# Performance work log

Measured on AMD Instinct MI355X. Metric: run time of the kernel, lower is better.

## Reference

```python
import jax, jax.numpy as jnp
import numpy as np
import math

D_MODEL, N_HEADS, BATCH, SEQ = 1024, 16, 2, 2048
D_HEAD = D_MODEL // N_HEADS


def setup_inputs() -> dict:
    key = jax.random.key(0)
    ks = jax.random.split(key, 5)
    w = lambda k: jax.random.normal(k, (D_MODEL, D_MODEL), jnp.float32) * 0.02
    return {
        "X": jax.random.normal(ks[0], (BATCH, SEQ, D_MODEL), jnp.float32),
        "W_q": w(ks[1]),
        "W_k": w(ks[2]),
        "W_v": w(ks[3]),
        "W_o": w(ks[4]),
        "g_q": jnp.ones((D_MODEL,), jnp.float32),
        "b_q": jnp.zeros((D_MODEL,), jnp.float32),
        "g_k": jnp.ones((D_MODEL,), jnp.float32),
        "b_k": jnp.zeros((D_MODEL,), jnp.float32),
        "cache_k": jnp.zeros((BATCH, N_HEADS, SEQ, D_HEAD), jnp.float32),
        "cache_v": jnp.zeros((BATCH, N_HEADS, SEQ, D_HEAD), jnp.float32),
        "start_pos": 0,
    }


def _layernorm(x, g, b, eps=1e-5):
    mu = jnp.mean(x, axis=-1, keepdims=True)
    xc = x - mu
    var = jnp.mean(xc * xc, axis=-1, keepdims=True)
    return xc * jax.lax.rsqrt(var + eps) * g + b


def reference(X, W_q, W_k, W_v, W_o, g_q, b_q, g_k, b_k, cache_k, cache_v, start_pos):
    batch, N, d_model = X.shape
    H = cache_k.shape[1]
    dh = d_model // H

    # QK-normed projections (torch Linear: x @ W^T)
    XQ = _layernorm(X @ W_q.T, g_q, b_q)
    XK = _layernorm(X @ W_k.T, g_k, b_k)
    XV = X @ W_v.T
    split = lambda t: t.reshape(batch, N, H, dh).transpose(0, 2, 1, 3)  # [b,h,n,d]
    XQ, XK, XV = split(XQ), split(XK), split(XV)

    # KV-cache scatter update, then slice to valid prefix (start_pos is static)
    cache_k = jax.lax.dynamic_update_slice(cache_k, XK, (0, 0, start_pos, 0))
    cache_v = jax.lax.dynamic_update_slice(cache_v, XV, (0, 0, start_pos, 0))
    M = start_pos + N
    K = cache_k[:, :, :M]
    V = cache_v[:, :, :M]

    logits = jnp.einsum('bhnd,bhmd->bhnm', XQ, K) / math.sqrt(dh)  # [b,h,N,M]

    # causal mask on the freshly written block [start_pos:M]
    tril = jnp.tril(jnp.ones((N, N), bool))
    full_mask = jnp.concatenate([jnp.ones((N, start_pos), bool), tril], axis=1)  # [N,M]
    logits = jnp.where(full_mask[None, None], logits, -jnp.inf)

    # selective forget-mask bias built from relu'd head-0 logits
    S = jax.nn.relu(logits[:, 0])               # relu(-inf) -> 0, matches torch
    S = S.at[..., 0].set(0.0)                   # zero first column
    S = S * (1.0 - jnp.eye(N, dtype=S.dtype))   # zero diagonal (valid since start_pos==0)
    S = jnp.roll(S, 1, axis=-2)                 # shift rows down by one
    S = S.at[..., 0, :].set(0.0)
    F_mask = jnp.cumsum(S, axis=-2)             # [b,N,M]

    logits = logits - F_mask[:, None]
    attn = jax.nn.softmax(logits, axis=-1)
    O = jnp.einsum('bhnm,bhmd->bhnd', attn, V)
    O = O.transpose(0, 2, 1, 3).reshape(batch, N, d_model)
    return O @ W_o.T
```

## Files before the change

kernel.cpp:

```cpp
#include <hip/hip_runtime.h>
#include <cstdint>
#include <cstddef>


typedef unsigned short u16;
typedef __attribute__((ext_vector_type(8))) __bf16 bf16x8;
typedef __attribute__((ext_vector_type(4))) float f32x4;

#define D_MODEL 1024
#define N_HEADS 16
#define BATCH   2
#define SEQ     2048
#define D_HEAD  64
#define ROWS    (BATCH*SEQ)
#define NSEG    64
#define SEGLEN  32
#define LOG2E   1.44269504f

static __device__ __forceinline__ u16 f2bf(float f){
  union { float f; uint32_t u; } v; v.f = f;
  uint32_t r = v.u + 0x7fffu + ((v.u >> 16) & 1u);
  return (u16)(r >> 16);
}
static __device__ __forceinline__ float bf2f(u16 h){
  union { uint32_t u; float f; } v; v.u = ((uint32_t)h) << 16;
  return v.f;
}
static __device__ __forceinline__ uint32_t pack2(float a, float b){
  uint32_t ua = __float_as_uint(a) + 0x8000u;
  uint32_t ub = __float_as_uint(b) + 0x8000u;
  return (ua >> 16) | (ub & 0xffff0000u);
}
#define GLDS(gp, lp) __builtin_amdgcn_global_load_lds( \
    (const __attribute__((address_space(1))) void*)(gp), \
    (__attribute__((address_space(3))) void*)(lp), 16, 0, 0)

__global__ void k_cast_all(const float* __restrict__ X,
                           u16* __restrict__ Xhi, u16* __restrict__ Xlo,
                           const float* __restrict__ Wq,
                           u16* __restrict__ Wqh, u16* __restrict__ Wql,
                           const float* __restrict__ Wk,
                           u16* __restrict__ Wkh, u16* __restrict__ Wkl,
                           const float* __restrict__ Wv, u16* __restrict__ Wvb,
                           const float* __restrict__ Wo, u16* __restrict__ Wob){
  int i = blockIdx.x*256 + threadIdx.x;
  if (i < 1572864){
    const float* src; u16 *dh, *dl; int base;
    if (i < 1048576){ src = X;  dh = Xhi; dl = Xlo; base = i; }
    else if (i < 1310720){ src = Wq; dh = Wqh; dl = Wql; base = i - 1048576; }
    else { src = Wk; dh = Wkh; dl = Wkl; base = i - 1310720; }
    float4 v = reinterpret_cast<const float4*>(src)[base];
    float vs[4] = {v.x, v.y, v.z, v.w};
    union { u16 s[4]; uint2 u; } uh, ul;
#pragma unroll
    for (int r=0;r<4;++r){
      uh.s[r] = f2bf(vs[r]);
      ul.s[r] = f2bf(vs[r] - bf2f(uh.s[r]));
    }
    reinterpret_cast<uint2*>(dh)[base] = uh.u;
    reinterpret_cast<uint2*>(dl)[base] = ul.u;
  } else {
    const float* src; u16* dst; int base;
    if (i < 1835008){ src = Wv; dst = Wvb; base = i - 1572864; }
    else { src = Wo; dst = Wob; base = i - 1835008; }
    float4 v = reinterpret_cast<const float4*>(src)[base];
    float vs[4] = {v.x, v.y, v.z, v.w};
    union { u16 s[4]; uint2 u; } uh;
#pragma unroll
    for (int r=0;r<4;++r) uh.s[r] = f2bf(vs[r]);
    reinterpret_cast<uint2*>(dst)[base] = uh.u;
  }
}

__global__ __launch_bounds__(256) void k_mega(
    const u16* __restrict__ Xhi, const u16* __restrict__ Xlo,
    const u16* __restrict__ Wh,  const u16* __restrict__ Wl,
    const u16* __restrict__ Wvb,
    float* __restrict__ C, float* __restrict__ Dlt, u16* __restrict__ Vt)
{
  __shared__ __align__(16) u16 smem[16384];
  const int bid = blockIdx.x;
  const int tid = threadIdx.x, wv = tid>>6, ln = tid&63;
  const int lane15 = ln&15, quad = ln>>4;
  const int wm = wv&1, wn = wv>>1;
  const int g = ln&7, sr = ln>>3;
  const int fs = lane15 & 7;
  f32x4 z = {0.f,0.f,0.f,0.f};
  u16* As = smem;
  u16* Bs = smem + 8192;

  if (bid < 128){
    const int cx = bid & 1;
    const int cy = (bid >> 1) & 31;
    const int cz = bid >> 6;
    const size_t rowBase = (size_t)cy*128;
    const size_t wbase = cx ? (size_t)1024*1024 : 0;
    const u16* Ap = cz ? Xlo : Xhi;
    const u16* Bp = (cz ? Wh : Wl) + wbase;
    f32x4 acc[4][2];
#pragma unroll
    for (int i=0;i<4;++i){ acc[i][0] = z; acc[i][1] = z; }
    for (int kt = 0; kt < 16; ++kt) {
      __syncthreads();
#pragma unroll
      for (int c = 0; c < 4; ++c) {
        int chunk = wv*4 + c, r = chunk*8 + sr;
        GLDS(Ap + (rowBase + r)*1024 + kt*64 + (g^sr)*8, As + chunk*512);
      }
#pragma unroll
      for (int c = 0; c < 2; ++c) {
        int chunk = wv*2 + c, r = chunk*8 + sr;
        GLDS(Bp + (size_t)r*1024 + kt*64 + (g^sr)*8, Bs + chunk*512);
      }
      __syncthreads();
#pragma unroll
      for (int k2=0;k2<2;++k2){
        bf16x8 af[4], bfb[2];
#pragma unroll
        for (int t=0;t<4;++t)
          af[t]  = *reinterpret_cast<const bf16x8*>(As + (wm*64 + t*16 + lane15)*64 + (((k2*4+quad)^fs)*8));
#pragma unroll
        for (int t=0;t<2;++t)
          bfb[t] = *reinterpret_cast<const bf16x8*>(Bs + (wn*32 + t*16 + lane15)*64 + (((k2*4+quad)^fs)*8));
#pragma unroll
        for (int i=0;i<4;++i)
#pragma unroll
          for (int j=0;j<2;++j)
            acc[i][j] = __builtin_amdgcn_mfma_f32_16x16x32_bf16(af[i], bfb[j], acc[i][j], 0,0,0);
      }
    }
#pragma unroll
    for (int i=0;i<4;++i){
      size_t row = rowBase + wm*64 + i*16 + quad*4;
#pragma unroll
      for (int j=0;j<2;++j){
        size_t col = (size_t)cx*64 + wn*32 + j*16 + lane15;
#pragma unroll
        for (int r=0;r<4;++r)
          atomicAdd(&Dlt[(row+r)*128 + col], acc[i][j][r]);
      }
    }
  } else if (bid < 640){
    const int idx = bid - 128;
    const size_t rowBase = (size_t)(idx>>4)*128, colBase = (size_t)(idx&15)*128;
    f32x4 acc[4][4];
#pragma unroll
    for (int i=0;i<4;++i)
#pragma unroll
      for (int j=0;j<4;++j) acc[i][j] = z;
    for (int kt = 0; kt < 16; ++kt) {
      __syncthreads();
#pragma unroll
      for (int c = 0; c < 4; ++c) {
        int chunk = wv*4 + c, r = chunk*8 + sr;
        GLDS(Xhi + (rowBase + r)*1024 + kt*64 + (g^sr)*8, As + chunk*512);
        GLDS(Wh  + (colBase + r)*1024 + kt*64 + (g^sr)*8, Bs + chunk*512);
      }
      __syncthreads();
#pragma unroll
      for (int k2=0;k2<2;++k2){
        bf16x8 af[4], bfb[4];
#pragma unroll
        for (int t=0;t<4;++t){
          af[t]  = *reinterpret_cast<const bf16x8*>(As + (wm*64 + t*16 + lane15)*64 + (((k2*4+quad)^fs)*8));
          bfb[t] = *reinterpret_cast<const bf16x8*>(Bs + (wn*64 + t*16 + lane15)*64 + (((k2*4+quad)^fs)*8));
        }
#pragma unroll
        for (int i=0;i<4;++i)
#pragma unroll
          for (int j=0;j<4;++j)
            acc[i][j] = __builtin_amdgcn_mfma_f32_16x16x32_bf16(af[i], bfb[j], acc[i][j], 0,0,0);
      }
    }
#pragma unroll
    for (int i=0;i<4;++i){
      size_t row = rowBase + wm*64 + i*16 + quad*4;
#pragma unroll
      for (int j=0;j<4;++j){
        size_t col = colBase + wn*64 + j*16 + lane15;
#pragma unroll
        for (int r=0;r<4;++r)
          C[(row+r)*2048 + col] = acc[i][j][r];
      }
    }
  } else {
    const int idx = bid - 640;
    const int bx = idx & 15, by = idx >> 4;
    const size_t rowBase = (size_t)by*128, colBase = (size_t)bx*64;
    f32x4 acc[4][2];
#pragma unroll
    for (int i=0;i<4;++i){ acc[i][0] = z; acc[i][1] = z; }
    for (int kt = 0; kt < 16; ++kt) {
      __syncthreads();
#pragma unroll
      for (int c = 0; c < 4; ++c) {
        int chunk = wv*4 + c, r = chunk*8 + sr;
        GLDS(Xhi + (rowBase + r)*1024 + kt*64 + (g^sr)*8, As + chunk*512);
      }
#pragma unroll
      for (int c = 0; c < 2; ++c) {
        int chunk = wv*2 + c, r = chunk*8 + sr;
        GLDS(Wvb + (colBase + r)*1024 + kt*64 + (g^sr)*8, Bs + chunk*512);
      }
      __syncthreads();
#pragma unroll
      for (int k2=0;k2<2;++k2){
        bf16x8 af[4], bfb[2];
#pragma unroll
        for (int t=0;t<4;++t)
          af[t]  = *reinterpret_cast<const bf16x8*>(As + (wm*64 + t*16 + lane15)*64 + (((k2*4+quad)^fs)*8));
#pragma unroll
        for (int t=0;t<2;++t)
          bfb[t] = *reinterpret_cast<const bf16x8*>(Bs + (wn*32 + t*16 + lane15)*64 + (((k2*4+quad)^fs)*8));
#pragma unroll
        for (int i=0;i<4;++i)
#pragma unroll
          for (int j=0;j<2;++j)
            acc[i][j] = __builtin_amdgcn_mfma_f32_16x16x32_bf16(af[i], bfb[j], acc[i][j], 0,0,0);
      }
    }
    __syncthreads();
#pragma unroll
    for (int i=0;i<4;++i){
      int nl = wm*64 + i*16 + quad*4;
#pragma unroll
      for (int j=0;j<2;++j){
        int dl = wn*32 + j*16 + lane15;
#pragma unroll
        for (int r=0;r<4;++r)
          smem[dl*136 + nl + r] = f2bf(acc[i][j][r]);
      }
    }
    __syncthreads();
    const int b = by >> 4;
    const int n0 = (by & 15) * 128;
    const int bh = b*N_HEADS + bx;
    const int d = tid >> 2, seg = tid & 3;
    u16* dst = Vt + ((size_t)(bh*64 + d))*SEQ + n0 + seg*32;
    const u16* srcl = smem + d*136 + seg*32;
#pragma unroll
    for (int k=0;k<4;++k)
      *reinterpret_cast<uint4*>(dst + k*8) = *reinterpret_cast<const uint4*>(srcl + k*8);
  }
}

__global__ __launch_bounds__(256) void k_ln_pack2(
    const float* __restrict__ C, const float* __restrict__ Dlt,
    const float* __restrict__ gq, const float* __restrict__ bq,
    const float* __restrict__ gk, const float* __restrict__ bk,
    u16* __restrict__ Qh, u16* __restrict__ Kh,
    u16* __restrict__ Q0l, u16* __restrict__ K0l)
{
  const int row = blockIdx.x;
  const int tid = threadIdx.x;
  const float* cr = C + (size_t)row*2048;
  float4 vq = reinterpret_cast<const float4*>(cr)[tid];
  float4 vk = reinterpret_cast<const float4*>(cr)[256 + tid];
  const int h = tid >> 4;
  if (h == 0){
    float4 dq = reinterpret_cast<const float4*>(Dlt + (size_t)row*128)[tid&15];
    vq.x+=dq.x; vq.y+=dq.y; vq.z+=dq.z; vq.w+=dq.w;
    float4 dk = reinterpret_cast<const float4*>(Dlt + (size_t)row*128 + 64)[tid&15];
    vk.x+=dk.x; vk.y+=dk.y; vk.z+=dk.z; vk.w+=dk.w;
  }
  float sq  = vq.x+vq.y+vq.z+vq.w;
  float s2q = vq.x*vq.x+vq.y*vq.y+vq.z*vq.z+vq.w*vq.w;
  float sk  = vk.x+vk.y+vk.z+vk.w;
  float s2k = vk.x*vk.x+vk.y*vk.y+vk.z*vk.z+vk.w*vk.w;
#pragma unroll
  for (int o=32;o;o>>=1){
    sq += __shfl_xor(sq,o);  s2q += __shfl_xor(s2q,o);
    sk += __shfl_xor(sk,o);  s2k += __shfl_xor(s2k,o);
  }
  __shared__ float red[4][4];
  if ((tid&63)==0){
    red[tid>>6][0]=sq; red[tid>>6][1]=s2q; red[tid>>6][2]=sk; red[tid>>6][3]=s2k;
  }
  __syncthreads();
  sq  = red[0][0]+red[1][0]+red[2][0]+red[3][0];
  s2q = red[0][1]+red[1][1]+red[2][1]+red[3][1];
  sk  = red[0][2]+red[1][2]+red[2][2]+red[3][2];
  s2k = red[0][3]+red[1][3]+red[2][3]+red[3][3];
  const float muq = sq*(1.f/D_MODEL);
  const float rsq = rsqrtf(s2q*(1.f/D_MODEL) - muq*muq + 1e-5f);
  const float muk = sk*(1.f/D_MODEL);
  const float rsk = rsqrtf(s2k*(1.f/D_MODEL) - muk*muk + 1e-5f);
  const int b = row >> 11, n = row & (SEQ-1);
  const int d0 = (tid & 15)*4;
  float4 gqv = reinterpret_cast<const float4*>(gq)[tid];
  float4 bqv = reinterpret_cast<const float4*>(bq)[tid];
  float4 gkv = reinterpret_cast<const float4*>(gk)[tid];
  float4 bkv = reinterpret_cast<const float4*>(bk)[tid];
  float xq[4] = {vq.x,vq.y,vq.z,vq.w}, xk[4] = {vk.x,vk.y,vk.z,vk.w};
  float gQ[4] = {gqv.x,gqv.y,gqv.z,gqv.w}, bQ[4] = {bqv.x,bqv.y,bqv.z,bqv.w};
  float gK[4] = {gkv.x,gkv.y,gkv.z,gkv.w}, bK[4] = {bkv.x,bkv.y,bkv.z,bkv.w};
  union { u16 s[4]; uint2 u; } qh, ql, kh, kl;
#pragma unroll
  for (int r=0;r<4;++r){
    float yq = (xq[r]-muq)*rsq*gQ[r] + bQ[r];
    qh.s[r] = f2bf(yq);
    ql.s[r] = f2bf(yq - bf2f(qh.s[r]));
    float yk = (xk[r]-muk)*rsk*gK[r] + bK[r];
    kh.s[r] = f2bf(yk);
    kl.s[r] = f2bf(yk - bf2f(kh.s[r]));
  }
  size_t dst = (((size_t)(b*N_HEADS + h))*SEQ + n)*D_HEAD + d0;
  *reinterpret_cast<uint2*>(Qh + dst) = qh.u;
  *reinterpret_cast<uint2*>(Kh + dst) = kh.u;
  if (h == 0){
    size_t dl = ((size_t)b*SEQ + n)*D_HEAD + d0;
    *reinterpret_cast<uint2*>(Q0l + dl) = ql.u;
    *reinterpret_cast<uint2*>(K0l + dl) = kl.u;
  }
}

__global__ __launch_bounds__(256) void k_s0(
    const u16* Qh, const u16* Q0l, const u16* Kh, const u16* K0l,
    float* __restrict__ S0, float* __restrict__ seg)
{
  const int b = blockIdx.z;
  const int bm = blockIdx.y;
  const int bn = blockIdx.x;
  const int tid = threadIdx.x;
  if (bn > bm){
    for (int t = tid; t < 512; t += 256)
      seg[((size_t)b*NSEG + bm*4 + (t>>7))*SEQ + bn*128 + (t&127)] = 0.f;
    return;
  }
  float* Sb = S0 + (size_t)b*SEQ*SEQ;
  __shared__ __align__(16) u16 smem[4*8192];
  const int wv = tid>>6, ln = tid&63;
  const int lane15 = ln&15, quad = ln>>4;
  const int wm = wv&1, wn = wv>>1;
  const int g = ln&7, sr = ln>>3;
  const int fs = lane15 & 7;
  const size_t rowBase = (size_t)bm*128, colBase = (size_t)bn*128;
  const u16* srcs[4] = {
    Qh  + ((size_t)b*N_HEADS*SEQ + rowBase)*D_HEAD,
    Q0l + ((size_t)b*SEQ + rowBase)*D_HEAD,
    Kh  + ((size_t)b*N_HEADS*SEQ + colBase)*D_HEAD,
    K0l + ((size_t)b*SEQ + colBase)*D_HEAD };
#pragma unroll
  for (int t=0;t<4;++t){
#pragma unroll
    for (int c=0;c<4;++c){
      int chunk = wv*4 + c, r = chunk*8 + sr;
      GLDS(srcs[t] + (size_t)r*64 + (g^sr)*8, smem + t*8192 + chunk*512);
    }
  }
  __syncthreads();
  f32x4 acc[4][4];
  f32x4 z = {0.f,0.f,0.f,0.f};
#pragma unroll
  for (int i=0;i<4;++i)
#pragma unroll
    for (int j=0;j<4;++j) acc[i][j] = z;
  const int Aidx[3] = {0, 0, 1};
  const int Bidx[3] = {2, 3, 2};
#pragma unroll
  for (int p = 0; p < 3; ++p){
    const u16* At = smem + Aidx[p]*8192;
    const u16* Bt = smem + Bidx[p]*8192;
#pragma unroll
    for (int k2=0;k2<2;++k2){
      bf16x8 af[4], bfb[4];
#pragma unroll
      for (int t=0;t<4;++t){
        af[t]  = *reinterpret_cast<const bf16x8*>(At + (wm*64 + t*16 + lane15)*64 + (((k2*4+quad)^fs)*8));
        bfb[t] = *reinterpret_cast<const bf16x8*>(Bt + (wn*64 + t*16 + lane15)*64 + (((k2*4+quad)^fs)*8));
      }
#pragma unroll
      for (int i=0;i<4;++i)
#pragma unroll
        for (int j=0;j<4;++j)
          acc[i][j] = __builtin_amdgcn_mfma_f32_16x16x32_bf16(af[i], bfb[j], acc[i][j], 0,0,0);
    }
  }
  float csum[2][4] = {{0.f,0.f,0.f,0.f},{0.f,0.f,0.f,0.f}};
#pragma unroll
  for (int i=0;i<4;++i){
#pragma unroll
    for (int j=0;j<4;++j){
#pragma unroll
      for (int r=0;r<4;++r){
        int jg = (int)rowBase + wm*64 + i*16 + quad*4 + r;
        int mg = (int)colBase + wn*64 + j*16 + lane15;
        float l = acc[i][j][r]*0.125f;
        float s = (mg >= 1 && mg < jg) ? fmaxf(l, 0.f) : 0.f;
        Sb[(size_t)jg*SEQ + mg] = s;
        csum[i>>1][j] += s;
      }
    }
  }
  __syncthreads();
  float* cs = (float*)smem;
#pragma unroll
  for (int h2=0;h2<2;++h2){
#pragma unroll
    for (int j=0;j<4;++j){
      float v = csum[h2][j];
      v += __shfl_xor(v, 16);
      v += __shfl_xor(v, 32);
      if (ln < 16) cs[(wm*2 + h2)*128 + wn*64 + j*16 + ln] = v;
    }
  }
  __syncthreads();
  for (int t = tid; t < 512; t += 256)
    seg[((size_t)b*NSEG + bm*4 + (t>>7))*SEQ + bn*128 + (t&127)] = cs[t];
}

__global__ void k_seg_apply(float* __restrict__ SF, const float* __restrict__ seg){
  int m = blockIdx.x*256 + threadIdx.x;
  int s = blockIdx.y, b = blockIdx.z;
  const float* sb = seg + (size_t)b*NSEG*SEQ;
  float run = 0.f;
  for (int t=0; t<s; ++t) run += sb[(size_t)t*SEQ + m];
  float* Sb = SF + (size_t)b*SEQ*SEQ;
  const int j0 = s*SEGLEN;
#pragma unroll 8
  for (int i=0;i<SEGLEN;++i){
    size_t idx = (size_t)(j0 + i)*SEQ + m;
    float t = Sb[idx];
    Sb[idx] = -run*LOG2E;
    run += (j0 + i > m) ? t : 0.f;
  }
}

__global__ __launch_bounds__(256, 4) void k_attn(
    const u16* __restrict__ Qh, const u16* __restrict__ Kh,
    const u16* __restrict__ Vt, const float* __restrict__ F,
    u16* __restrict__ Ob)
{
  __shared__ __align__(16) u16 Ks[2][64*64];
  __shared__ __align__(16) u16 Vs[2][64*64];
  const int h = blockIdx.x, b = blockIdx.z;
  const int nt = b ? (int)(gridDim.y - 1 - blockIdx.y) : (int)blockIdx.y;
  const int tid = threadIdx.x, wv = tid>>6, ln = tid&63;
  const int lane15 = ln&15, quad = ln>>4;
  const u16* Qbh = Qh + ((size_t)(b*N_HEADS + h))*SEQ*D_HEAD;
  const u16* Kbh = Kh + ((size_t)(b*N_HEADS + h))*SEQ*D_HEAD;
  const u16* Vbh = Vt + ((size_t)(b*N_HEADS + h))*D_HEAD*SEQ;
  const int n_loc = wv*16 + lane15;
  const int n_g = nt*64 + n_loc;
  const float* Frow = F + (size_t)b*SEQ*SEQ + (size_t)n_g*SEQ;
  const int swz = (ln&7) ^ ((ln>>3)&7);
  const int fswz = lane15 & 7;
  const int srow = ln>>3;

  bf16x8 qf[2];
#pragma unroll
  for (int kt=0; kt<2; ++kt)
    qf[kt] = *reinterpret_cast<const bf16x8*>(Qbh + (size_t)n_g*D_HEAD + kt*32 + quad*8);

  f32x4 z = {0.f,0.f,0.f,0.f};
  f32x4 psum = z;
  f32x4 acc_o[4];
#pragma unroll
  for (int no=0;no<4;++no) acc_o[no] = z;

  auto stage = [&](int mt, int buf){
#pragma unroll
    for (int c=0;c<2;++c){
      int chunk = wv*2 + c;
      int r = chunk*8 + srow;
      GLDS(Kbh + (size_t)(mt*64 + r)*D_HEAD + swz*8, &Ks[buf][chunk*512]);
      GLDS(Vbh + (size_t)r*SEQ + mt*64 + swz*8,      &Vs[buf][chunk*512]);
    }
  };
  stage(0, 0);
  f32x4 fvn[4];
#pragma unroll
  for (int ms=0; ms<4; ++ms)
    fvn[ms] = *reinterpret_cast<const f32x4*>(Frow + ms*16 + quad*4);
  const float c1 = 0.125f*LOG2E;

  for (int mt = 0; mt <= nt; ++mt) {
    const int cur = mt & 1;
    __syncthreads();
    if (mt < nt) stage(mt+1, 1-cur);
    f32x4 fv[4];
#pragma unroll
    for (int ms=0; ms<4; ++ms) fv[ms] = fvn[ms];
    if (mt < nt){
      const float* Fr1 = Frow + (mt+1)*64;
#pragma unroll
      for (int ms=0; ms<4; ++ms)
        fvn[ms] = *reinterpret_cast<const f32x4*>(Fr1 + ms*16 + quad*4);
    }
    f32x4 accs[4];
#pragma unroll
    for (int ms=0;ms<4;++ms) accs[ms] = z;
#pragma unroll
    for (int kt=0; kt<2; ++kt){
#pragma unroll
      for (int ms=0; ms<4; ++ms){
        bf16x8 a = *reinterpret_cast<const bf16x8*>(
            &Ks[cur][(ms*16 + lane15)*64 + (((kt*4 + quad) ^ fswz) * 8)]);
        accs[ms] = __builtin_amdgcn_mfma_f32_16x16x32_bf16(a, qf[kt], accs[ms], 0,0,0);
      }
    }
    const bool diag = (mt == nt);
    uint32_t pw[4][2];
#pragma unroll
    for (int ms=0; ms<4; ++ms){
      f32x4 t = accs[ms];
      float p[4];
#pragma unroll
      for (int r=0;r<4;++r){
        float l2 = fmaf(t[r], c1, fv[ms][r]);
        if (diag){
          int ml = ms*16 + quad*4 + r;
          l2 = (ml > n_loc) ? -1e30f : l2;
        }
        p[r] = __builtin_amdgcn_exp2f(l2);
      }
      psum[0]+=p[0]; psum[1]+=p[1]; psum[2]+=p[2]; psum[3]+=p[3];
      pw[ms][0] = pack2(p[0], p[1]);
      pw[ms][1] = pack2(p[2], p[3]);
    }
#pragma unroll
    for (int kt=0; kt<2; ++kt){
      union { uint32_t u[4]; bf16x8 v; } pa;
#pragma unroll
      for (int w=0; w<4; ++w){
        int sl = lane15 + 16*((quad&1)*2 + (w>>1));
        uint32_t t0 = (uint32_t)__shfl((int)pw[2*kt  ][w&1], sl);
        uint32_t t1 = (uint32_t)__shfl((int)pw[2*kt+1][w&1], sl);
        pa.u[w] = (quad < 2) ? t0 : t1;
      }
#pragma unroll
      for (int no=0; no<4; ++no){
        int d = no*16 + lane15;
        bf16x8 vb = *reinterpret_cast<const bf16x8*>(
            &Vs[cur][d*64 + (((kt*4 + quad) ^ (d&7)) * 8)]);
        acc_o[no] = __builtin_amdgcn_mfma_f32_16x16x32_bf16(pa.v, vb, acc_o[no], 0,0,0);
      }
    }
  }
  float s = (psum[0]+psum[1]) + (psum[2]+psum[3]);
  s += __shfl_xor(s, 16);
  s += __shfl_xor(s, 32);
  f32x4 inv;
#pragma unroll
  for (int r=0;r<4;++r)
    inv[r] = __builtin_amdgcn_rcpf(__shfl(s, quad*4 + r));
#pragma unroll
  for (int no=0; no<4; ++no){
#pragma unroll
    for (int r=0;r<4;++r){
      float o = acc_o[no][r] * inv[r];
      int row = nt*64 + wv*16 + quad*4 + r;
      Ob[((size_t)(b*SEQ + row))*D_MODEL + h*64 + no*16 + lane15] = f2bf(o);
    }
  }
}

__global__ __launch_bounds__(256) void k_gemm_nt64(
    const u16* __restrict__ A0, const u16* __restrict__ B0,
    float* __restrict__ C, int N, int K)
{
  __shared__ __align__(16) u16 As[8192];
  __shared__ __align__(16) u16 Bs[4096];
  const int tid = threadIdx.x, wv = tid>>6, ln = tid&63;
  const int lane15 = ln&15, quad = ln>>4;
  const int wm = wv&1, wn = wv>>1;
  const int g = ln&7, sr = ln>>3;
  const int fs = lane15 & 7;
  const size_t rowBase = (size_t)blockIdx.y*128, colBase = (size_t)blockIdx.x*64;
  f32x4 acc[4][2];
  f32x4 z = {0.f,0.f,0.f,0.f};
#pragma unroll
  for (int i=0;i<4;++i){ acc[i][0] = z; acc[i][1] = z; }
  const int ktiles = K >> 6;
  for (int kt = 0; kt < ktiles; ++kt) {
    __syncthreads();
#pragma unroll
    for (int c = 0; c < 4; ++c) {
      int chunk = wv*4 + c, r = chunk*8 + sr;
      GLDS(A0 + (rowBase + r)*K + kt*64 + (g^sr)*8, As + chunk*512);
    }
#pragma unroll
    for (int c = 0; c < 2; ++c) {
      int chunk = wv*2 + c, r = chunk*8 + sr;
      GLDS(B0 + (colBase + r)*K + kt*64 + (g^sr)*8, Bs + chunk*512);
    }
    __syncthreads();
#pragma unroll
    for (int k2=0;k2<2;++k2){
      bf16x8 af[4], bfb[2];
#pragma unroll
      for (int t=0;t<4;++t)
        af[t]  = *reinterpret_cast<const bf16x8*>(As + (wm*64 + t*16 + lane15)*64 + (((k2*4+quad)^fs)*8));
#pragma unroll
      for (int t=0;t<2;++t)
        bfb[t] = *reinterpret_cast<const bf16x8*>(Bs + (wn*32 + t*16 + lane15)*64 + (((k2*4+quad)^fs)*8));
#pragma unroll
      for (int i=0;i<4;++i)
#pragma unroll
        for (int j=0;j<2;++j)
          acc[i][j] = __builtin_amdgcn_mfma_f32_16x16x32_bf16(af[i], bfb[j], acc[i][j], 0,0,0);
    }
  }
#pragma unroll
  for (int i=0;i<4;++i){
    size_t row = rowBase + wm*64 + i*16 + quad*4;
#pragma unroll
    for (int j=0;j<2;++j){
      size_t col = colBase + wn*32 + j*16 + lane15;
#pragma unroll
      for (int r=0;r<4;++r)
        C[(row+r)*N + col] = acc[i][j][r];
    }
  }
}

extern "C" void kernel_launch(void* const* d_in, const int* in_sizes, int n_in,
                              void* d_out, int out_size, void* d_ws, size_t ws_size,
                              hipStream_t stream)
{
  (void)in_sizes; (void)n_in; (void)out_size; (void)ws_size;
  const float* X  = (const float*)d_in[0];
  const float* Wq = (const float*)d_in[1];
  const float* Wk = (const float*)d_in[2];
  const float* Wv = (const float*)d_in[3];
  const float* Wo = (const float*)d_in[4];
  const float* gq = (const float*)d_in[5];
  const float* bq = (const float*)d_in[6];
  const float* gk = (const float*)d_in[7];
  const float* bk = (const float*)d_in[8];
  float* out = (float*)d_out;

  char* ws = (char*)d_ws;
  size_t off = 0;
  auto alloc = [&](size_t bytes)->char*{
    char* p = ws + off; off += (bytes + 255) & ~(size_t)255; return p;
  };
  u16* Xhi  = (u16*)alloc((size_t)ROWS*D_MODEL*2);
  u16* Xlo  = (u16*)alloc((size_t)ROWS*D_MODEL*2);
  u16* Wqkh = (u16*)alloc((size_t)2*D_MODEL*D_MODEL*2);
  u16* Wqkl = (u16*)alloc((size_t)2*D_MODEL*D_MODEL*2);
  u16* Wvb  = (u16*)alloc((size_t)D_MODEL*D_MODEL*2);
  u16* Wob  = (u16*)alloc((size_t)D_MODEL*D_MODEL*2);
  u16* Qhp  = (u16*)alloc((size_t)BATCH*N_HEADS*SEQ*D_HEAD*2);
  u16* Khp  = (u16*)alloc((size_t)BATCH*N_HEADS*SEQ*D_HEAD*2);
  u16* Q0l  = (u16*)alloc((size_t)BATCH*SEQ*D_HEAD*2);
  u16* K0l  = (u16*)alloc((size_t)BATCH*SEQ*D_HEAD*2);
  u16* Vtp  = (u16*)alloc((size_t)BATCH*N_HEADS*D_HEAD*SEQ*2);
  u16* Obf  = (u16*)alloc((size_t)ROWS*D_MODEL*2);
  float* Dlt = (float*)alloc((size_t)ROWS*128*4);
  float* Seg = (float*)alloc((size_t)BATCH*NSEG*SEQ*4);
  float* SF  = (float*)alloc((size_t)BATCH*SEQ*SEQ*4);
  float* C32 = SF;

  hipMemsetAsync(Dlt, 0, (size_t)ROWS*128*4, stream);

  k_cast_all<<<8192, 256, 0, stream>>>(
      X, Xhi, Xlo,
      Wq, Wqkh, Wqkl,
      Wk, Wqkh + (size_t)D_MODEL*D_MODEL, Wqkl + (size_t)D_MODEL*D_MODEL,
      Wv, Wvb, Wo, Wob);
  k_mega<<<1152, 256, 0, stream>>>(Xhi, Xlo, Wqkh, Wqkl, Wvb, C32, Dlt, Vtp);
  k_ln_pack2<<<ROWS, 256, 0, stream>>>(C32, Dlt, gq, bq, gk, bk, Qhp, Khp, Q0l, K0l);
  k_s0<<<dim3(16, 16, BATCH), 256, 0, stream>>>(Qhp, Q0l, Khp, K0l, SF, Seg);
  k_seg_apply<<<dim3(8, NSEG, BATCH), 256, 0, stream>>>(SF, Seg);
  k_attn<<<dim3(N_HEADS, SEQ/64, BATCH), 256, 0, stream>>>(Qhp, Khp, Vtp, SF, Obf);
  k_gemm_nt64<<<dim3(16, 32), 256, 0, stream>>>(Obf, Wob, out, D_MODEL, D_MODEL);
}
```

Before: 292.3 us.

## Pair complementary causal query tiles per attention block to balance work and reuse K/V

Each attention block now handles two query tiles, ta and 31-ta, so every block does the same total causal work. The K/V tiles staged in shared memory are reused by both tiles' MFMAs, which halves the grid and the K/V loads per unit of work. Register pressure doubles (two sets of accumulators and Q fragments), so launch bounds drop to 2 waves per EU, which risks lower occupancy and less latency hiding.

New measurement: 302.7 us. 3.5% more time.

```diff
diff --git a/kernel.cpp b/kernel.cpp
--- a/kernel.cpp
+++ b/kernel.cpp
@@ -426,7 +426,7 @@
   }
 }
 
-__global__ __launch_bounds__(256, 4) void k_attn(
+__global__ __launch_bounds__(256, 2) void k_attn(
     const u16* __restrict__ Qh, const u16* __restrict__ Kh,
     const u16* __restrict__ Vt, const float* __restrict__ F,
     u16* __restrict__ Ob)
@@ -434,29 +434,34 @@
   __shared__ __align__(16) u16 Ks[2][64*64];
   __shared__ __align__(16) u16 Vs[2][64*64];
   const int h = blockIdx.x, b = blockIdx.z;
-  const int nt = b ? (int)(gridDim.y - 1 - blockIdx.y) : (int)blockIdx.y;
+  const int ta = blockIdx.y;
+  const int tb = 31 - ta;
   const int tid = threadIdx.x, wv = tid>>6, ln = tid&63;
   const int lane15 = ln&15, quad = ln>>4;
   const u16* Qbh = Qh + ((size_t)(b*N_HEADS + h))*SEQ*D_HEAD;
   const u16* Kbh = Kh + ((size_t)(b*N_HEADS + h))*SEQ*D_HEAD;
   const u16* Vbh = Vt + ((size_t)(b*N_HEADS + h))*D_HEAD*SEQ;
   const int n_loc = wv*16 + lane15;
-  const int n_g = nt*64 + n_loc;
-  const float* Frow = F + (size_t)b*SEQ*SEQ + (size_t)n_g*SEQ;
+  const int nA = ta*64 + n_loc, nB = tb*64 + n_loc;
+  const float* FrowA = F + (size_t)b*SEQ*SEQ + (size_t)nA*SEQ;
+  const float* FrowB = F + (size_t)b*SEQ*SEQ + (size_t)nB*SEQ;
   const int swz = (ln&7) ^ ((ln>>3)&7);
   const int fswz = lane15 & 7;
   const int srow = ln>>3;
-
-  bf16x8 qf[2];
-#pragma unroll
-  for (int kt=0; kt<2; ++kt)
-    qf[kt] = *reinterpret_cast<const bf16x8*>(Qbh + (size_t)n_g*D_HEAD + kt*32 + quad*8);
+  const float c1 = 0.125f*LOG2E;
+
+  bf16x8 qfA[2], qfB[2];
+#pragma unroll
+  for (int kt=0; kt<2; ++kt){
+    qfA[kt] = *reinterpret_cast<const bf16x8*>(Qbh + (size_t)nA*D_HEAD + kt*32 + quad*8);
+    qfB[kt] = *reinterpret_cast<const bf16x8*>(Qbh + (size_t)nB*D_HEAD + kt*32 + quad*8);
+  }
 
   f32x4 z = {0.f,0.f,0.f,0.f};
-  f32x4 psum = z;
-  f32x4 acc_o[4];
-#pragma unroll
-  for (int no=0;no<4;++no) acc_o[no] = z;
+  f32x4 psumA = z, psumB = z;
+  f32x4 accoA[4], accoB[4];
+#pragma unroll
+  for (int no=0;no<4;++no){ accoA[no] = z; accoB[no] = z; }
 
   auto stage = [&](int mt, int buf){
 #pragma unroll
@@ -468,91 +473,117 @@
     }
   };
   stage(0, 0);
-  f32x4 fvn[4];
-#pragma unroll
-  for (int ms=0; ms<4; ++ms)
-    fvn[ms] = *reinterpret_cast<const f32x4*>(Frow + ms*16 + quad*4);
-  const float c1 = 0.125f*LOG2E;
-
-  for (int mt = 0; mt <= nt; ++mt) {
+  f32x4 fvnA[4], fvnB[4];
+#pragma unroll
+  for (int ms=0; ms<4; ++ms){
+    fvnA[ms] = *reinterpret_cast<const f32x4*>(FrowA + ms*16 + quad*4);
+    fvnB[ms] = *reinterpret_cast<const f32x4*>(FrowB + ms*16 + quad*4);
+  }
+
+  auto smax = [&](const f32x4* accs, const f32x4* fv, f32x4& psum,
+                  uint32_t (*pw)[2], bool diag){
+#pragma unroll
+    for (int ms=0; ms<4; ++ms){
+      f32x4 t = accs[ms];
+      float p[4];
+#pragma unroll
+      for (int r=0;r<4;++r){
+        float l2 = fmaf(t[r], c1, fv[ms][r]);
+        int ml = ms*16 + quad*4 + r;
+        l2 = (diag && ml > n_loc) ? -1e30f : l2;
+        p[r] = __builtin_amdgcn_exp2f(l2);
+      }
+      psum[0]+=p[0]; psum[1]+=p[1]; psum[2]+=p[2]; psum[3]+=p[3];
+      pw[ms][0] = pack2(p[0], p[1]);
+      pw[ms][1] = pack2(p[2], p[3]);
+    }
+  };
+  auto build_pa = [&](const uint32_t (*pw)[2], int kt)->bf16x8{
+    union { uint32_t u[4]; bf16x8 v; } pa;
+#pragma unroll
+    for (int w=0; w<4; ++w){
+      int sl = lane15 + 16*((quad&1)*2 + (w>>1));
+      uint32_t t0 = (uint32_t)__shfl((int)pw[2*kt  ][w&1], sl);
+      uint32_t t1 = (uint32_t)__shfl((int)pw[2*kt+1][w&1], sl);
+      pa.u[w] = (quad < 2) ? t0 : t1;
+    }
+    return pa.v;
+  };
+
+  for (int mt = 0; mt <= tb; ++mt) {
     const int cur = mt & 1;
     __syncthreads();
-    if (mt < nt) stage(mt+1, 1-cur);
-    f32x4 fv[4];
-#pragma unroll
-    for (int ms=0; ms<4; ++ms) fv[ms] = fvn[ms];
-    if (mt < nt){
-      const float* Fr1 = Frow + (mt+1)*64;
+    if (mt < tb) stage(mt+1, 1-cur);
+    const bool doA = (mt <= ta);
+    f32x4 fvA[4], fvB[4];
+#pragma unroll
+    for (int ms=0; ms<4; ++ms){ fvA[ms] = fvnA[ms]; fvB[ms] = fvnB[ms]; }
+    if (mt < tb){
+      const float* Fr1 = FrowB + (mt+1)*64;
 #pragma unroll
       for (int ms=0; ms<4; ++ms)
-        fvn[ms] = *reinterpret_cast<const f32x4*>(Fr1 + ms*16 + quad*4);
-    }
-    f32x4 accs[4];
-#pragma unroll
-    for (int ms=0;ms<4;++ms) accs[ms] = z;
+        fvnB[ms] = *reinterpret_cast<const f32x4*>(Fr1 + ms*16 + quad*4);
+    }
+    if (mt < ta){
+      const float* Fr1 = FrowA + (mt+1)*64;
+#pragma unroll
+      for (int ms=0; ms<4; ++ms)
+        fvnA[ms] = *reinterpret_cast<const f32x4*>(Fr1 + ms*16 + quad*4);
+    }
+    f32x4 accsA[4], accsB[4];
+#pragma unroll
+    for (int ms=0;ms<4;++ms){ accsA[ms] = z; accsB[ms] = z; }
 #pragma unroll
     for (int kt=0; kt<2; ++kt){
 #pragma unroll
       for (int ms=0; ms<4; ++ms){
         bf16x8 a = *reinterpret_cast<const bf16x8*>(
             &Ks[cur][(ms*16 + lane15)*64 + (((kt*4 + quad) ^ fswz) * 8)]);
-        accs[ms] = __builtin_amdgcn_mfma_f32_16x16x32_bf16(a, qf[kt], accs[ms], 0,0,0);
-      }
-    }
-    const bool diag = (mt == nt);
-    uint32_t pw[4][2];
-#pragma unroll
-    for (int ms=0; ms<4; ++ms){
-      f32x4 t = accs[ms];
-      float p[4];
-#pragma unroll
-      for (int r=0;r<4;++r){
-        float l2 = fmaf(t[r], c1, fv[ms][r]);
-        if (diag){
-          int ml = ms*16 + quad*4 + r;
-          l2 = (ml > n_loc) ? -1e30f : l2;
-        }
-        p[r] = __builtin_amdgcn_exp2f(l2);
-      }
-      psum[0]+=p[0]; psum[1]+=p[1]; psum[2]+=p[2]; psum[3]+=p[3];
-      pw[ms][0] = pack2(p[0], p[1]);
-      pw[ms][1] = pack2(p[2], p[3]);
-    }
+        accsB[ms] = __builtin_amdgcn_mfma_f32_16x16x32_bf16(a, qfB[kt], accsB[ms], 0,0,0);
+        if (doA)
+          accsA[ms] = __builtin_amdgcn_mfma_f32_16x16x32_bf16(a, qfA[kt], accsA[ms], 0,0,0);
+      }
+    }
+    uint32_t pwA[4][2], pwB[4][2];
+    smax(accsB, fvB, psumB, pwB, mt == tb);
+    if (doA) smax(accsA, fvA, psumA, pwA, mt == ta);
 #pragma unroll
     for (int kt=0; kt<2; ++kt){
-      union { uint32_t u[4]; bf16x8 v; } pa;
-#pragma unroll
-      for (int w=0; w<4; ++w){
-        int sl = lane15 + 16*((quad&1)*2 + (w>>1));
-        uint32_t t0 = (uint32_t)__shfl((int)pw[2*kt  ][w&1], sl);
-        uint32_t t1 = (uint32_t)__shfl((int)pw[2*kt+1][w&1], sl);
-        pa.u[w] = (quad < 2) ? t0 : t1;
-      }
+      bf16x8 paB = build_pa(pwB, kt);
+      bf16x8 paA;
+      if (doA) paA = build_pa(pwA, kt);
 #pragma unroll
       for (int no=0; no<4; ++no){
         int d = no*16 + lane15;
         bf16x8 vb = *reinterpret_cast<const bf16x8*>(
             &Vs[cur][d*64 + (((kt*4 + quad) ^ (d&7)) * 8)]);
-        acc_o[no] = __builtin_amdgcn_mfma_f32_16x16x32_bf16(pa.v, vb, acc_o[no], 0,0,0);
-      }
-    }
-  }
-  float s = (psum[0]+psum[1]) + (psum[2]+psum[3]);
-  s += __shfl_xor(s, 16);
-  s += __shfl_xor(s, 32);
-  f32x4 inv;
-#pragma unroll
-  for (int r=0;r<4;++r)
-    inv[r] = __builtin_amdgcn_rcpf(__shfl(s, quad*4 + r));
-#pragma unroll
-  for (int no=0; no<4; ++no){
-#pragma unroll
-    for (int r=0;r<4;++r){
-      float o = acc_o[no][r] * inv[r];
-      int row = nt*64 + wv*16 + quad*4 + r;
-      Ob[((size_t)(b*SEQ + row))*D_MODEL + h*64 + no*16 + lane15] = f2bf(o);
-    }
-  }
+        accoB[no] = __builtin_amdgcn_mfma_f32_16x16x32_bf16(paB, vb, accoB[no], 0,0,0);
+        if (doA)
+          accoA[no] = __builtin_amdgcn_mfma_f32_16x16x32_bf16(paA, vb, accoA[no], 0,0,0);
+      }
+    }
+  }
+
+  auto finalize = [&](const f32x4& psum, const f32x4* acc_o, int tt){
+    float s = (psum[0]+psum[1]) + (psum[2]+psum[3]);
+    s += __shfl_xor(s, 16);
+    s += __shfl_xor(s, 32);
+    f32x4 inv;
+#pragma unroll
+    for (int r=0;r<4;++r)
+      inv[r] = __builtin_amdgcn_rcpf(__shfl(s, quad*4 + r));
+#pragma unroll
+    for (int no=0; no<4; ++no){
+#pragma unroll
+      for (int r=0;r<4;++r){
+        float o = acc_o[no][r] * inv[r];
+        int row = tt*64 + wv*16 + quad*4 + r;
+        Ob[((size_t)(b*SEQ + row))*D_MODEL + h*64 + no*16 + lane15] = f2bf(o);
+      }
+    }
+  };
+  finalize(psumB, accoB, tb);
+  finalize(psumA, accoA, ta);
 }
 
 __global__ __launch_bounds__(256) void k_gemm_nt64(
@@ -663,6 +694,6 @@
   k_ln_pack2<<<ROWS, 256, 0, stream>>>(C32, Dlt, gq, bq, gk, bk, Qhp, Khp, Q0l, K0l);
   k_s0<<<dim3(16, 16, BATCH), 256, 0, stream>>>(Qhp, Q0l, Khp, K0l, SF, Seg);
   k_seg_apply<<<dim3(8, NSEG, BATCH), 256, 0, stream>>>(SF, Seg);
-  k_attn<<<dim3(N_HEADS, SEQ/64, BATCH), 256, 0, stream>>>(Qhp, Khp, Vtp, SF, Obf);
+  k_attn<<<dim3(N_HEADS, 16, BATCH), 256, 0, stream>>>(Qhp, Khp, Vtp, SF, Obf);
   k_gemm_nt64<<<dim3(16, 32), 256, 0, stream>>>(Obf, Wob, out, D_MODEL, D_MODEL);
 }
```

## Split long causal attention row tiles into two KV halves with combine kernel

Applied to the files above, without the earlier changes.

Row tiles 16..31 of the causal attention are now split into two work items over halves of the key range. This balances per-block work, and a static map orders blocks longest-first for better load balance across CUs. Partial unnormalized outputs and row sums go to a float workspace, and a new combine kernel adds them and normalizes to bf16. This is safe without max rescaling because the softmax here has no running max. It adds an extra kernel launch and extra global traffic for the partial results.

Result: no change. 292.3 us (-0.0%).

```diff
diff --git a/kernel.cpp b/kernel.cpp
--- a/kernel.cpp
+++ b/kernel.cpp
@@ -426,15 +426,37 @@
   }
 }
 
+__constant__ unsigned char WMAP[48] = {
+  62,63,60,79,
+  61,58,59,56,78,
+  57,54,55,52,77,
+  53,50,51,48,76,
+  49,46,47,44,75,
+  45,42,43,40,74,
+  41,38,39,36,73,
+  37,34,35,32,72,
+  33,71,
+  70,69,68,67,66,65,64};
+
 __global__ __launch_bounds__(256, 4) void k_attn(
     const u16* __restrict__ Qh, const u16* __restrict__ Kh,
     const u16* __restrict__ Vt, const float* __restrict__ F,
-    u16* __restrict__ Ob)
+    u16* __restrict__ Ob, float* __restrict__ Opart, float* __restrict__ Ps)
 {
   __shared__ __align__(16) u16 Ks[2][64*64];
   __shared__ __align__(16) u16 Vs[2][64*64];
-  const int h = blockIdx.x, b = blockIdx.z;
-  const int nt = b ? (int)(gridDim.y - 1 - blockIdx.y) : (int)blockIdx.y;
+  const int w = blockIdx.x;
+  const int bh = w & 31, b = bh >> 4, h = bh & 15;
+  const int item = (int)WMAP[w >> 5];
+  int nt, mt0, mt1, segi;
+  if (item >= 64){ nt = item - 64; segi = 0; mt0 = 0; mt1 = nt; }
+  else {
+    nt = item >> 1; segi = item & 1;
+    const int half = (nt + 2) >> 1;
+    mt0 = segi ? half : 0;
+    mt1 = segi ? nt : (half - 1);
+  }
+  const bool partial = (item < 64);
   const int tid = threadIdx.x, wv = tid>>6, ln = tid&63;
   const int lane15 = ln&15, quad = ln>>4;
   const u16* Qbh = Qh + ((size_t)(b*N_HEADS + h))*SEQ*D_HEAD;
@@ -467,21 +489,21 @@
       GLDS(Vbh + (size_t)r*SEQ + mt*64 + swz*8,      &Vs[buf][chunk*512]);
     }
   };
-  stage(0, 0);
+  stage(mt0, mt0 & 1);
   f32x4 fvn[4];
 #pragma unroll
   for (int ms=0; ms<4; ++ms)
-    fvn[ms] = *reinterpret_cast<const f32x4*>(Frow + ms*16 + quad*4);
+    fvn[ms] = *reinterpret_cast<const f32x4*>(Frow + mt0*64 + ms*16 + quad*4);
   const float c1 = 0.125f*LOG2E;
 
-  for (int mt = 0; mt <= nt; ++mt) {
+  for (int mt = mt0; mt <= mt1; ++mt) {
     const int cur = mt & 1;
     __syncthreads();
-    if (mt < nt) stage(mt+1, 1-cur);
+    if (mt < mt1) stage(mt+1, 1-cur);
     f32x4 fv[4];
 #pragma unroll
     for (int ms=0; ms<4; ++ms) fv[ms] = fvn[ms];
-    if (mt < nt){
+    if (mt < mt1){
       const float* Fr1 = Frow + (mt+1)*64;
 #pragma unroll
       for (int ms=0; ms<4; ++ms)
@@ -522,11 +544,11 @@
     for (int kt=0; kt<2; ++kt){
       union { uint32_t u[4]; bf16x8 v; } pa;
 #pragma unroll
-      for (int w=0; w<4; ++w){
-        int sl = lane15 + 16*((quad&1)*2 + (w>>1));
-        uint32_t t0 = (uint32_t)__shfl((int)pw[2*kt  ][w&1], sl);
-        uint32_t t1 = (uint32_t)__shfl((int)pw[2*kt+1][w&1], sl);
-        pa.u[w] = (quad < 2) ? t0 : t1;
+      for (int wq=0; wq<4; ++wq){
+        int sl = lane15 + 16*((quad&1)*2 + (wq>>1));
+        uint32_t t0 = (uint32_t)__shfl((int)pw[2*kt  ][wq&1], sl);
+        uint32_t t1 = (uint32_t)__shfl((int)pw[2*kt+1][wq&1], sl);
+        pa.u[wq] = (quad < 2) ? t0 : t1;
       }
 #pragma unroll
       for (int no=0; no<4; ++no){
@@ -540,19 +562,58 @@
   float s = (psum[0]+psum[1]) + (psum[2]+psum[3]);
   s += __shfl_xor(s, 16);
   s += __shfl_xor(s, 32);
-  f32x4 inv;
-#pragma unroll
-  for (int r=0;r<4;++r)
-    inv[r] = __builtin_amdgcn_rcpf(__shfl(s, quad*4 + r));
-#pragma unroll
-  for (int no=0; no<4; ++no){
-#pragma unroll
-    for (int r=0;r<4;++r){
-      float o = acc_o[no][r] * inv[r];
-      int row = nt*64 + wv*16 + quad*4 + r;
-      Ob[((size_t)(b*SEQ + row))*D_MODEL + h*64 + no*16 + lane15] = f2bf(o);
-    }
-  }
+  if (partial){
+    const size_t pb = (size_t)(bh*16 + (nt - 16))*2 + segi;
+    float* Op = Opart + pb*4096;
+    if (quad == 0) Ps[pb*64 + wv*16 + lane15] = s;
+#pragma unroll
+    for (int no=0; no<4; ++no)
+#pragma unroll
+      for (int r=0;r<4;++r)
+        Op[(wv*16 + quad*4 + r)*64 + no*16 + lane15] = acc_o[no][r];
+  } else {
+    f32x4 inv;
+#pragma unroll
+    for (int r=0;r<4;++r)
+      inv[r] = __builtin_amdgcn_rcpf(__shfl(s, quad*4 + r));
+#pragma unroll
+    for (int no=0; no<4; ++no){
+#pragma unroll
+      for (int r=0;r<4;++r){
+        float o = acc_o[no][r] * inv[r];
+        int row = nt*64 + wv*16 + quad*4 + r;
+        Ob[((size_t)(b*SEQ + row))*D_MODEL + h*64 + no*16 + lane15] = f2bf(o);
+      }
+    }
+  }
+}
+
+__global__ __launch_bounds__(256) void k_comb(
+    const float* __restrict__ Opart, const float* __restrict__ Ps,
+    u16* __restrict__ Ob)
+{
+  const int t = blockIdx.x;
+  const int bh = t >> 4, b = bh >> 4, h = bh & 15;
+  const int nt = (t & 15) + 16;
+  const int tid = threadIdx.x;
+  const int row = tid >> 2, c0 = (tid & 3) * 16;
+  const float* P0 = Opart + (size_t)t*2*4096 + row*64 + c0;
+  const float* P1 = P0 + 4096;
+  const float s = Ps[(size_t)t*128 + row] + Ps[(size_t)t*128 + 64 + row];
+  const float inv = __builtin_amdgcn_rcpf(s);
+  union { u16 us[16]; uint4 u[2]; } o;
+#pragma unroll
+  for (int g2=0; g2<4; ++g2){
+    float4 a = reinterpret_cast<const float4*>(P0)[g2];
+    float4 c = reinterpret_cast<const float4*>(P1)[g2];
+    o.us[g2*4+0] = f2bf((a.x + c.x) * inv);
+    o.us[g2*4+1] = f2bf((a.y + c.y) * inv);
+    o.us[g2*4+2] = f2bf((a.z + c.z) * inv);
+    o.us[g2*4+3] = f2bf((a.w + c.w) * inv);
+  }
+  u16* dst = Ob + ((size_t)(b*SEQ + nt*64 + row))*D_MODEL + h*64 + c0;
+  reinterpret_cast<uint4*>(dst)[0] = o.u[0];
+  reinterpret_cast<uint4*>(dst)[1] = o.u[1];
 }
 
 __global__ __launch_bounds__(256) void k_gemm_nt64(
@@ -649,6 +710,8 @@
   u16* Obf  = (u16*)alloc((size_t)ROWS*D_MODEL*2);
   float* Dlt = (float*)alloc((size_t)ROWS*128*4);
   float* Seg = (float*)alloc((size_t)BATCH*NSEG*SEQ*4);
+  float* Opart = (float*)alloc((size_t)512*2*4096*4);
+  float* Ps    = (float*)alloc((size_t)512*2*64*4);
   float* SF  = (float*)alloc((size_t)BATCH*SEQ*SEQ*4);
   float* C32 = SF;
 
@@ -663,6 +726,7 @@
   k_ln_pack2<<<ROWS, 256, 0, stream>>>(C32, Dlt, gq, bq, gk, bk, Qhp, Khp, Q0l, K0l);
   k_s0<<<dim3(16, 16, BATCH), 256, 0, stream>>>(Qhp, Q0l, Khp, K0l, SF, Seg);
   k_seg_apply<<<dim3(8, NSEG, BATCH), 256, 0, stream>>>(SF, Seg);
-  k_attn<<<dim3(N_HEADS, SEQ/64, BATCH), 256, 0, stream>>>(Qhp, Khp, Vtp, SF, Obf);
+  k_attn<<<1536, 256, 0, stream>>>(Qhp, Khp, Vtp, SF, Obf, Opart, Ps);
+  k_comb<<<512, 256, 0, stream>>>(Opart, Ps, Obf);
   k_gemm_nt64<<<dim3(16, 32), 256, 0, stream>>>(Obf, Wob, out, D_MODEL, D_MODEL);
 }
```
